# Performance work log

Measured on AMD Instinct MI355X. Metric: run time of the kernel, lower is better.

Reference implementation:

```python
import jax, jax.numpy as jnp
import numpy as np

H = 1024          # hidden_size
A = 8             # num_actions
T = 64            # timesteps
N = 256           # batch (num envs)


def _gru_cell(x, h, Wih, Whh, bih, bhh):
    # torch.nn.GRUCell math; gate order (r, z, n)
    gi = x @ Wih.T + bih           # [N, 3H]
    gh = h @ Whh.T + bhh           # [N, 3H]
    i_r, i_z, i_n = jnp.split(gi, 3, axis=1)
    h_r, h_z, h_n = jnp.split(gh, 3, axis=1)
    r = jax.nn.sigmoid(i_r + h_r)
    z = jax.nn.sigmoid(i_z + h_z)
    n = jnp.tanh(i_n + r * h_n)
    return (1.0 - z) * n + z * h


def setup_inputs() -> dict:
    key = jax.random.key(0)
    ks = jax.random.split(key, 12)
    s = 0.02
    return {
        "c": jax.random.normal(ks[0], (T * N, H), jnp.float32),
        "hxs": jax.random.normal(ks[1], (N, 3 * H), jnp.float32),
        "masks": jnp.ones((T * N, 1), jnp.float32),
        "prev_action_one_hot": jnp.zeros((T * N, A), jnp.float32).at[jnp.arange(T * N), jax.random.randint(ks[2], (T * N,), 0, A)].set(1.0),
        "h_gru_Wih": s * jax.random.normal(ks[3], (3 * H, H), jnp.float32),
        "h_gru_Whh": s * jax.random.normal(ks[4], (3 * H, H), jnp.float32),
        "h_gru_bih": jnp.zeros((3 * H,), jnp.float32),
        "h_gru_bhh": jnp.zeros((3 * H,), jnp.float32),
        "f_gru_Wih": s * jax.random.normal(ks[5], (3 * H, H), jnp.float32),
        "f_gru_Whh": s * jax.random.normal(ks[6], (3 * H, H), jnp.float32),
        "f_gru_bih": jnp.zeros((3 * H,), jnp.float32),
        "f_gru_bhh": jnp.zeros((3 * H,), jnp.float32),
        "p_W": s * jax.random.normal(ks[7], (2 * H, 2 * H + A), jnp.float32),
        "p_b": jnp.zeros((2 * H,), jnp.float32),
        "q_W": s * jax.random.normal(ks[8], (2 * H, 2 * H + A), jnp.float32),
        "q_b": jnp.zeros((2 * H,), jnp.float32),
    }


def reference(c, hxs, masks, prev_action_one_hot,
              h_gru_Wih, h_gru_Whh, h_gru_bih, h_gru_bhh,
              f_gru_Wih, f_gru_Whh, f_gru_bih, f_gru_bhh,
              p_W, p_b, q_W, q_b):
    c3 = c.reshape(T, N, H)
    m3 = masks.reshape(T, N, 1)
    a3 = prev_action_one_hot.reshape(T, N, A)
    f0 = hxs[:, :H]
    h0 = hxs[:, H:2 * H]
    q0 = hxs[:, 2 * H:]

    def step(carry, xs):
        f, h, q_mu = carry
        c_t, m_t, a_t = xs
        p_in = jnp.concatenate([h, q_mu, a_t], axis=1) * m_t
        p_dist = p_in @ p_W.T + p_b                     # [N, 2H]
        p_mu = p_dist[:, :H]
        q_in = jnp.concatenate([f, c_t, a_t], axis=1) * m_t
        q_dist = q_in @ q_W.T + q_b                     # [N, 2H]
        q_mu_new = q_dist[:, :H]
        f_new = _gru_cell(c_t, f * m_t, f_gru_Wih, f_gru_Whh, f_gru_bih, f_gru_bhh)
        h_new = _gru_cell(p_mu, h * m_t, h_gru_Wih, h_gru_Whh, h_gru_bih, h_gru_bhh)
        return (f_new, h_new, q_mu_new), (p_dist, q_dist)

    (f, h, q_mu), (p_all, q_all) = jax.lax.scan(step, (f0, h0, q0), (c3, m3, a3))
    acc_p = p_all.reshape(T * N, 2 * H)
    acc_q = q_all.reshape(T * N, 2 * H)
    hxs_out = jnp.concatenate([f, h, q_mu], axis=1)
    return acc_p, acc_q, hxs_out
```

## Files before the change

kernel.cpp:

```cpp
#include <hip/hip_runtime.h>
#include <math.h>

typedef __attribute__((ext_vector_type(8))) __bf16 bf16x8;
typedef __attribute__((ext_vector_type(4))) float f32x4;

constexpr int H = 1024, T = 64, NB = 256, TWOH = 2048, THREEH = 3072;
constexpr long long OFF_Q  = 33554432LL;
constexpr long long OFF_HX = 67108864LL;
constexpr int LA = 6;

constexpr int R_PWH = 0, R_PWQ = 2048, R_QWF = 4096, R_QWC = 6144,
              R_FWIH = 8192, R_FWHH = 11264, R_HWIH = 14336, R_HWHH = 17408;

#define LD4(p) (*reinterpret_cast<const float4*>(p))

__device__ __forceinline__ float sigf(float x) { return 1.0f / (1.0f + expf(-x)); }

__device__ __forceinline__ void gload16(const void* g, void* l) {
    __builtin_amdgcn_global_load_lds(
        (const __attribute__((address_space(1))) uint32_t*)g,
        (__attribute__((address_space(3))) uint32_t*)l, 16, 0, 0);
}

__device__ __forceinline__ void st_bf_swz(__bf16* base, int n, int k, float v) {
    base[(size_t)n * 1024 + (((k >> 3) ^ (n & 7)) << 3) + (k & 7)] = (__bf16)v;
}

__device__ __forceinline__ void swz_rc(int i, int NR, int& rt, int& ct) {
    const int k = i & 7;
    const int m = i >> 3;
    ct = k + 8 * (m / NR);
    rt = m % NR;
}

#define FRAGOFF(rloc, gl) (((rloc) << 7) + ((((gl)) ^ ((rloc) & 7)) << 4))

template<int RT>
__device__ __forceinline__ void stage_tile(const char* g, char* l, int kb, int tid) {
    #pragma unroll
    for (int i = 0; i < RT / 32; ++i) {
        const int L = i * 4096 + tid * 16;
        gload16(g + (size_t)(L >> 7) * 2048 + (size_t)kb * 128 + (L & 127), l + L);
    }
}

__device__ __forceinline__ void mm128(
    int tid, char* sA, char* sB,
    const char* A, const char* B,
    f32x4 (&acc)[2][4])
{
    const int lane = tid & 63, w = tid >> 6;
    const int l15 = lane & 15, lg = lane >> 4;
    const int wr = w >> 1, wc = w & 1;
    int aoff[2][2], boff[4][2];
    #pragma unroll
    for (int fr = 0; fr < 2; ++fr)
        #pragma unroll
        for (int kk = 0; kk < 2; ++kk)
            aoff[fr][kk] = FRAGOFF(wr * 32 + fr * 16 + l15, kk * 4 + lg);
    #pragma unroll
    for (int fc = 0; fc < 4; ++fc)
        #pragma unroll
        for (int kk = 0; kk < 2; ++kk)
            boff[fc][kk] = FRAGOFF(wc * 64 + fc * 16 + l15, kk * 4 + lg);

    stage_tile<64>(A, sA, 0, tid);
    stage_tile<128>(B, sB, 0, tid);
    stage_tile<64>(A, sA + 8192, 1, tid);
    stage_tile<128>(B, sB + 16384, 1, tid);
    for (int kb = 0; kb < 16; ++kb) {
        const int kn = kb + 2;
        if (kn < 16) {
            const int bo = kn % 3;
            stage_tile<64>(A, sA + bo * 8192, kn, tid);
            stage_tile<128>(B, sB + bo * 16384, kn, tid);
            asm volatile("s_waitcnt vmcnt(12)" ::: "memory");
        } else if (kb + 1 < 16) {
            asm volatile("s_waitcnt vmcnt(6)" ::: "memory");
        } else {
            asm volatile("s_waitcnt vmcnt(0)" ::: "memory");
        }
        __builtin_amdgcn_s_barrier();
        __builtin_amdgcn_sched_barrier(0);
        const int bc = kb % 3;
        char* Ab = sA + bc * 8192;
        char* Bb = sB + bc * 16384;
        bf16x8 af[2][2], bv[4][2];
        #pragma unroll
        for (int fr = 0; fr < 2; ++fr)
            #pragma unroll
            for (int kk = 0; kk < 2; ++kk)
                af[fr][kk] = *reinterpret_cast<const bf16x8*>(Ab + aoff[fr][kk]);
        #pragma unroll
        for (int fc = 0; fc < 4; ++fc)
            #pragma unroll
            for (int kk = 0; kk < 2; ++kk)
                bv[fc][kk] = *reinterpret_cast<const bf16x8*>(Bb + boff[fc][kk]);
        __builtin_amdgcn_s_setprio(1);
        #pragma unroll
        for (int kk = 0; kk < 2; ++kk)
            #pragma unroll
            for (int fr = 0; fr < 2; ++fr)
                #pragma unroll
                for (int fc = 0; fc < 4; ++fc)
                    acc[fr][fc] = __builtin_amdgcn_mfma_f32_16x16x32_bf16(
                        af[fr][kk], bv[fc][kk], acc[fr][fc], 0, 0, 0);
        __builtin_amdgcn_s_setprio(0);
        __builtin_amdgcn_s_barrier();
        __builtin_amdgcn_sched_barrier(0);
    }
}

__device__ __forceinline__ void mm32g1(
    int tid, char* sA, char* sB,
    const char* A, const char* Bg,
    f32x4 (&aR)[2], f32x4 (&aZ)[2], f32x4 (&aN)[2])
{
    const int lane = tid & 63, w = tid >> 6;
    const int l15 = lane & 15, lg = lane >> 4;
    const int wr = w >> 1, wc = w & 1;
    int aoff[2], boff[2][2];
    #pragma unroll
    for (int kk = 0; kk < 2; ++kk)
        aoff[kk] = FRAGOFF(wr * 16 + l15, kk * 4 + lg);
    #pragma unroll
    for (int fc = 0; fc < 2; ++fc)
        #pragma unroll
        for (int kk = 0; kk < 2; ++kk)
            boff[fc][kk] = FRAGOFF(wc * 32 + fc * 16 + l15, kk * 4 + lg);

    auto stg = [&](int buf, int kb) {
        stage_tile<32>(A, sA + buf * 4096, kb, tid);
        #pragma unroll
        for (int g = 0; g < 3; ++g)
            stage_tile<64>(Bg + (size_t)g * 2097152, sB + buf * 24576 + g * 8192, kb, tid);
    };
    stg(0, 0);
    for (int kb = 0; kb < 16; ++kb) {
        if (kb + 1 < 16) {
            stg((kb + 1) & 1, kb + 1);
            asm volatile("s_waitcnt vmcnt(7)" ::: "memory");
        } else {
            asm volatile("s_waitcnt vmcnt(0)" ::: "memory");
        }
        __builtin_amdgcn_s_barrier();
        __builtin_amdgcn_sched_barrier(0);
        char* Ab = sA + (kb & 1) * 4096;
        char* Bb = sB + (kb & 1) * 24576;
        bf16x8 af[2];
        #pragma unroll
        for (int kk = 0; kk < 2; ++kk)
            af[kk] = *reinterpret_cast<const bf16x8*>(Ab + aoff[kk]);
        bf16x8 bvr[2][2], bvz[2][2], bvn[2][2];
        #pragma unroll
        for (int fc = 0; fc < 2; ++fc)
            #pragma unroll
            for (int kk = 0; kk < 2; ++kk) {
                bvr[fc][kk] = *reinterpret_cast<const bf16x8*>(Bb + boff[fc][kk]);
                bvz[fc][kk] = *reinterpret_cast<const bf16x8*>(Bb + 8192 + boff[fc][kk]);
                bvn[fc][kk] = *reinterpret_cast<const bf16x8*>(Bb + 16384 + boff[fc][kk]);
            }
        __builtin_amdgcn_s_setprio(1);
        #pragma unroll
        for (int kk = 0; kk < 2; ++kk)
            #pragma unroll
            for (int fc = 0; fc < 2; ++fc) {
                aR[fc] = __builtin_amdgcn_mfma_f32_16x16x32_bf16(af[kk], bvr[fc][kk], aR[fc], 0, 0, 0);
                aZ[fc] = __builtin_amdgcn_mfma_f32_16x16x32_bf16(af[kk], bvz[fc][kk], aZ[fc], 0, 0, 0);
                aN[fc] = __builtin_amdgcn_mfma_f32_16x16x32_bf16(af[kk], bvn[fc][kk], aN[fc], 0, 0, 0);
            }
        __builtin_amdgcn_s_setprio(0);
        __builtin_amdgcn_s_barrier();
        __builtin_amdgcn_sched_barrier(0);
    }
}

__device__ __forceinline__ void do_xq(int slice, int i, int tid, char* sA, char* sB,
    const char* cbfB, const char* Wb, const float* act, const float* qW, float* out)
{
    const int lane = tid & 63, w = tid >> 6;
    const int l15 = lane & 15, lg = lane >> 4;
    const int wr = w >> 1, wc = w & 1;
    int rt, ct; swz_rc(i, 4, rt, ct);
    const int row0 = rt * 64, col0 = ct * 128;
    const size_t grow0 = (size_t)slice * NB + row0;
    f32x4 acc[2][4] = {};
    mm128(tid, sA, sB, cbfB + grow0 * 2048, Wb + (size_t)(R_QWC + col0) * 2048, acc);
    #pragma unroll
    for (int fc = 0; fc < 4; ++fc) {
        const int gc = col0 + wc * 64 + fc * 16 + l15;
        const float* wp = qW + (size_t)gc * 2056 + 2048;
        float4 x0 = LD4(wp), x1 = LD4(wp + 4);
        #pragma unroll
        for (int fr = 0; fr < 2; ++fr)
            #pragma unroll
            for (int j = 0; j < 4; ++j) {
                const size_t n = grow0 + wr * 32 + fr * 16 + lg * 4 + j;
                const float* ar = act + n * 8;
                float4 a0 = LD4(ar), a1 = LD4(ar + 4);
                float dot = a0.x * x0.x + a0.y * x0.y + a0.z * x0.z + a0.w * x0.w
                          + a1.x * x1.x + a1.y * x1.y + a1.z * x1.z + a1.w * x1.w;
                out[OFF_Q + n * TWOH + gc] = acc[fr][fc][j] + dot;
            }
    }
}

__device__ __forceinline__ void do_gf(int slice, int i, int tid, char* sA, char* sB,
    const char* cbfB, const char* Wb, __bf16* Gfb)
{
    const int lane = tid & 63, w = tid >> 6;
    const int l15 = lane & 15, lg = lane >> 4;
    const int wr = w >> 1, wc = w & 1;
    int rt, ct; swz_rc(i, 4, rt, ct);
    const int row0 = rt * 64, col0 = ct * 128;
    f32x4 acc[2][4] = {};
    mm128(tid, sA, sB, cbfB + ((size_t)slice * NB + row0) * 2048,
          Wb + (size_t)(R_FWIH + col0) * 2048, acc);
    __bf16* gdst = Gfb + (size_t)(slice & 7) * NB * THREEH;
    #pragma unroll
    for (int fc = 0; fc < 4; ++fc) {
        const int gc = col0 + wc * 64 + fc * 16 + l15;
        #pragma unroll
        for (int fr = 0; fr < 2; ++fr)
            #pragma unroll
            for (int j = 0; j < 4; ++j) {
                const int n = row0 + wr * 32 + fr * 16 + lg * 4 + j;
                gdst[(size_t)n * THREEH + gc] = (__bf16)acc[fr][fc][j];
            }
    }
}

__device__ __forceinline__ void do_pq(int tt, int i, int tid, char* sA, char* sB,
    const __bf16* qmu_t, const char* Wb, const float* masks, const float* act,
    const float* pW, const float* pb, float* out)
{
    const int lane = tid & 63, w = tid >> 6;
    const int l15 = lane & 15, lg = lane >> 4;
    const int wr = w >> 1, wc = w & 1;
    int rt, ct; swz_rc(i, 4, rt, ct);
    const int row0 = rt * 64, col0 = ct * 128;
    f32x4 acc[2][4] = {};
    mm128(tid, sA, sB, (const char*)qmu_t + (size_t)row0 * 2048,
          Wb + (size_t)(R_PWQ + col0) * 2048, acc);
    const float* mrow = masks + (size_t)tt * NB;
    float* ob = out + (size_t)tt * NB * TWOH;
    #pragma unroll
    for (int fc = 0; fc < 4; ++fc) {
        const int gc = col0 + wc * 64 + fc * 16 + l15;
        const float* wp = pW + (size_t)gc * 2056 + 2048;
        float4 x0 = LD4(wp), x1 = LD4(wp + 4);
        const float bb = pb[gc];
        #pragma unroll
        for (int fr = 0; fr < 2; ++fr)
            #pragma unroll
            for (int j = 0; j < 4; ++j) {
                const int n = row0 + wr * 32 + fr * 16 + lg * 4 + j;
                const float* ar = act + ((size_t)tt * NB + n) * 8;
                float4 a0 = LD4(ar), a1 = LD4(ar + 4);
                float dot = a0.x * x0.x + a0.y * x0.y + a0.z * x0.z + a0.w * x0.w
                          + a1.x * x1.x + a1.y * x1.y + a1.z * x1.z + a1.w * x1.w;
                ob[(size_t)n * TWOH + gc] = acc[fr][fc][j] + mrow[n] * dot + bb;
            }
    }
}

__global__ __launch_bounds__(256) void wcvt_k(
    const float* __restrict__ pW, const float* __restrict__ qW,
    const float* __restrict__ fWih, const float* __restrict__ fWhh,
    const float* __restrict__ hWih, const float* __restrict__ hWhh,
    __bf16* __restrict__ Wbf)
{
    const long i = (long)blockIdx.x * 256 + threadIdx.x;
    const int row = (int)(i >> 7);
    const int G   = (int)i & 127;
    const float* src; int stride; int koff = 0; int r;
    if (row < 2048)       { src = pW;   stride = 2056; koff = 0;    r = row; }
    else if (row < 4096)  { src = pW;   stride = 2056; koff = 1024; r = row - 2048; }
    else if (row < 6144)  { src = qW;   stride = 2056; koff = 0;    r = row - 4096; }
    else if (row < 8192)  { src = qW;   stride = 2056; koff = 1024; r = row - 6144; }
    else if (row < 11264) { src = fWih; stride = 1024; r = row - 8192; }
    else if (row < 14336) { src = fWhh; stride = 1024; r = row - 11264; }
    else if (row < 17408) { src = hWih; stride = 1024; r = row - 14336; }
    else                  { src = hWhh; stride = 1024; r = row - 17408; }
    const float* p = src + (long)r * stride + koff + G * 8;
    float4 a = LD4(p), b = LD4(p + 4);
    bf16x8 v;
    v[0] = (__bf16)a.x; v[1] = (__bf16)a.y; v[2] = (__bf16)a.z; v[3] = (__bf16)a.w;
    v[4] = (__bf16)b.x; v[5] = (__bf16)b.y; v[6] = (__bf16)b.z; v[7] = (__bf16)b.w;
    *reinterpret_cast<bf16x8*>(Wbf + (size_t)row * 1024 + ((G ^ (row & 7)) << 3)) = v;
}

__global__ __launch_bounds__(256) void ccvt_k(const float* __restrict__ c,
                                              __bf16* __restrict__ cbf) {
    const long i = (long)blockIdx.x * 256 + threadIdx.x;
    const int row = (int)(i >> 7);
    const int G   = (int)i & 127;
    const float* p = c + (size_t)row * 1024 + G * 8;
    float4 a = LD4(p), b = LD4(p + 4);
    bf16x8 v;
    v[0] = (__bf16)a.x; v[1] = (__bf16)a.y; v[2] = (__bf16)a.z; v[3] = (__bf16)a.w;
    v[4] = (__bf16)b.x; v[5] = (__bf16)b.y; v[6] = (__bf16)b.z; v[7] = (__bf16)b.w;
    *reinterpret_cast<bf16x8*>(cbf + (size_t)row * 1024 + ((G ^ (row & 7)) << 3)) = v;
}

__global__ __launch_bounds__(256) void init2_k(
    const float* __restrict__ hxs, const float* __restrict__ masks,
    float* __restrict__ fst0, float* __restrict__ hst0,
    __bf16* __restrict__ fbm0, __bf16* __restrict__ hbm0, __bf16* __restrict__ qmub0)
{
    const int idx = blockIdx.x * 256 + threadIdx.x;
    const int arr = idx >> 15;
    const int g   = idx & 32767;
    const int n   = g >> 7;
    const int G   = g & 127;
    const float m0 = masks[n];
    const float* p = hxs + (size_t)n * THREEH + arr * 1024 + G * 8;
    float4 a = LD4(p), b = LD4(p + 4);
    __bf16* dstB = arr == 0 ? fbm0 : (arr == 1 ? hbm0 : qmub0);
    bf16x8 v;
    v[0] = (__bf16)(a.x * m0); v[1] = (__bf16)(a.y * m0);
    v[2] = (__bf16)(a.z * m0); v[3] = (__bf16)(a.w * m0);
    v[4] = (__bf16)(b.x * m0); v[5] = (__bf16)(b.y * m0);
    v[6] = (__bf16)(b.z * m0); v[7] = (__bf16)(b.w * m0);
    *reinterpret_cast<bf16x8*>(dstB + (size_t)n * 1024 + ((G ^ (n & 7)) << 3)) = v;
    if (arr < 2) {
        float* dstF = arr == 0 ? fst0 : hst0;
        *reinterpret_cast<float4*>(dstF + (size_t)n * 1024 + G * 8) = a;
        *reinterpret_cast<float4*>(dstF + (size_t)n * 1024 + G * 8 + 4) = b;
    }
}

__global__ __launch_bounds__(256) void pre_k(
    const char* __restrict__ cbfB, const char* __restrict__ Wb,
    const float* __restrict__ act, const float* __restrict__ qW,
    const __bf16* __restrict__ qmb0, const float* __restrict__ masks,
    const float* __restrict__ pW, const float* __restrict__ pb,
    __bf16* __restrict__ Gfb, float* __restrict__ out)
{
    __shared__ char smem[73728];
    if (blockIdx.x < LA * 160) {
        const int s = blockIdx.x / 160;
        const int i = blockIdx.x % 160;
        if (i < 64) do_xq(s, i, threadIdx.x, smem, smem + 24576, cbfB, Wb, act, qW, out);
        else        do_gf(s, i - 64, threadIdx.x, smem, smem + 24576, cbfB, Wb, Gfb);
    } else {
        do_pq(0, blockIdx.x - LA * 160, threadIdx.x, smem, smem + 24576,
              qmb0, Wb, masks, act, pW, pb, out);
    }
}

__global__ __launch_bounds__(256) void k1_k(
    int t,
    const __bf16* __restrict__ hbm, const __bf16* __restrict__ fbm,
    __bf16* __restrict__ qmubN,
    const float* __restrict__ masks, const float* __restrict__ act,
    const float* __restrict__ qb, const float* __restrict__ qW,
    const char* __restrict__ Wb,
    __bf16* __restrict__ pmub, float* __restrict__ Shh,
    const __bf16* __restrict__ Gfb,
    const float* __restrict__ fbih, const float* __restrict__ fbhh,
    const float* __restrict__ fstF, float* __restrict__ fstN, __bf16* __restrict__ fbmN,
    float* __restrict__ out)
{
    __shared__ char smem[73728];
    char* sA = smem;
    char* sB = smem + 24576;
    const int tid = threadIdx.x;
    const int lane = tid & 63, w = tid >> 6;
    const int l15 = lane & 15, lg = lane >> 4;
    const int wr = w >> 1, wc = w & 1;
    const float* mrow = masks + (size_t)t * NB;
    const float* mn   = masks + (size_t)(t + 1 < T ? t + 1 : t) * NB;
    int b = blockIdx.x;

    if (b < 64) {
        int rt, ct; swz_rc(b, 4, rt, ct);
        const int row0 = rt * 64, col0 = ct * 128;
        f32x4 acc[2][4] = {};
        mm128(tid, sA, sB, (const char*)hbm + (size_t)row0 * 2048,
              Wb + (size_t)(R_PWH + col0) * 2048, acc);
        float* ob = out + (size_t)t * NB * TWOH;
        #pragma unroll
        for (int fc = 0; fc < 4; ++fc) {
            const int gc = col0 + wc * 64 + fc * 16 + l15;
            #pragma unroll
            for (int fr = 0; fr < 2; ++fr)
                #pragma unroll
                for (int j = 0; j < 4; ++j) {
                    const int n = row0 + wr * 32 + fr * 16 + lg * 4 + j;
                    const float v = ob[(size_t)n * TWOH + gc] + acc[fr][fc][j];
                    ob[(size_t)n * TWOH + gc] = v;
                    if (gc < 1024) st_bf_swz(pmub, n, gc, v);
                }
        }
    } else if (b < 128) {
        int rt, ct; swz_rc(b - 64, 4, rt, ct);
        const int row0 = rt * 64, col0 = ct * 128;
        f32x4 acc[2][4] = {};
        mm128(tid, sA, sB, (const char*)fbm + (size_t)row0 * 2048,
              Wb + (size_t)(R_QWF + col0) * 2048, acc);
        float* ob = out + OFF_Q + (size_t)t * NB * TWOH;
        #pragma unroll
        for (int fc = 0; fc < 4; ++fc) {
            const int gc = col0 + wc * 64 + fc * 16 + l15;
            const float bb = qb[gc];
            #pragma unroll
            for (int fr = 0; fr < 2; ++fr)
                #pragma unroll
                for (int j = 0; j < 4; ++j) {
                    const int n = row0 + wr * 32 + fr * 16 + lg * 4 + j;
                    const float xq = ob[(size_t)n * TWOH + gc];
                    float v = acc[fr][fc][j] + mrow[n] * xq + bb;
                    ob[(size_t)n * TWOH + gc] = v;
                    if (gc < 1024) st_bf_swz(qmubN, n, gc, v * mn[n]);
                }
        }
    } else if (b < 224) {
        int rt, ct; swz_rc(b - 128, 4, rt, ct);
        const int row0 = rt * 64, col0 = ct * 128;
        f32x4 acc[2][4] = {};
        mm128(tid, sA, sB, (const char*)hbm + (size_t)row0 * 2048,
              Wb + (size_t)(R_HWHH + col0) * 2048, acc);
        #pragma unroll
        for (int fc = 0; fc < 4; ++fc) {
            const int gc = col0 + wc * 64 + fc * 16 + l15;
            #pragma unroll
            for (int fr = 0; fr < 2; ++fr)
                #pragma unroll
                for (int j = 0; j < 4; ++j) {
                    const int n = row0 + wr * 32 + fr * 16 + lg * 4 + j;
                    Shh[(size_t)n * THREEH + gc] = acc[fr][fc][j];
                }
        }
    } else {
        int rt, ct; swz_rc(b - 224, 8, rt, ct);
        const int row0 = rt * 32, col0 = ct * 64;
        f32x4 aR[2] = {}, aZ[2] = {}, aN[2] = {};
        mm32g1(tid, sA, sB, (const char*)fbm + (size_t)row0 * 2048,
               Wb + (size_t)(R_FWHH + col0) * 2048, aR, aZ, aN);
        const __bf16* gsl = Gfb + (size_t)(t & 7) * NB * THREEH;
        #pragma unroll
        for (int fc = 0; fc < 2; ++fc) {
            const int col = col0 + wc * 32 + fc * 16 + l15;
            const float br  = fbih[col] + fbhh[col];
            const float bz  = fbih[col + 1024] + fbhh[col + 1024];
            const float bni = fbih[col + 2048], bnh = fbhh[col + 2048];
            #pragma unroll
            for (int j = 0; j < 4; ++j) {
                const int n = row0 + wr * 16 + lg * 4 + j;
                const float gfr = (float)gsl[(size_t)n * THREEH + col];
                const float gfz = (float)gsl[(size_t)n * THREEH + col + 1024];
                const float gfn = (float)gsl[(size_t)n * THREEH + col + 2048];
                const float rg = sigf(gfr + aR[fc][j] + br);
                const float zg = sigf(gfz + aZ[fc][j] + bz);
                const float ng = tanhf(gfn + bni + rg * (aN[fc][j] + bnh));
                const float fm = fstF[(size_t)n * 1024 + col] * mrow[n];
                const float o = (1.f - zg) * ng + zg * fm;
                fstN[(size_t)n * 1024 + col] = o;
                st_bf_swz(fbmN, n, col, o * mn[n]);
            }
        }
    }
}

__global__ __launch_bounds__(256) void k2_k(
    int t,
    const __bf16* __restrict__ pmub, const __bf16* __restrict__ qmubN,
    const char* __restrict__ cbfB,
    const float* __restrict__ Shh,
    const float* __restrict__ hstF, float* __restrict__ hstN, __bf16* __restrict__ hbmN,
    const char* __restrict__ Wb,
    const float* __restrict__ hbih, const float* __restrict__ hbhh,
    const float* __restrict__ masks, const float* __restrict__ act,
    const float* __restrict__ pW, const float* __restrict__ pb,
    const float* __restrict__ qW,
    __bf16* __restrict__ Gfb, float* __restrict__ out)
{
    __shared__ char smem[73728];
    char* sA = smem;
    char* sB = smem + 24576;
    const int tid = threadIdx.x;
    const int lane = tid & 63, w = tid >> 6;
    const int l15 = lane & 15, lg = lane >> 4;
    const int wr = w >> 1, wc = w & 1;
    const float* mrow = masks + (size_t)t * NB;
    const float* mn   = masks + (size_t)(t + 1 < T ? t + 1 : t) * NB;
    const int b = blockIdx.x;

    if (b < 128) {
        int rt, ct; swz_rc(b, 8, rt, ct);
        const int row0 = rt * 32, col0 = ct * 64;
        f32x4 aR[2] = {}, aZ[2] = {}, aN[2] = {};
        mm32g1(tid, sA, sB, (const char*)pmub + (size_t)row0 * 2048,
               Wb + (size_t)(R_HWIH + col0) * 2048, aR, aZ, aN);
        #pragma unroll
        for (int fc = 0; fc < 2; ++fc) {
            const int col = col0 + wc * 32 + fc * 16 + l15;
            const float bri = hbih[col],        brh = hbhh[col];
            const float bzi = hbih[col + 1024], bzh = hbhh[col + 1024];
            const float bni = hbih[col + 2048], bnh = hbhh[col + 2048];
            #pragma unroll
            for (int j = 0; j < 4; ++j) {
                const int n = row0 + wr * 16 + lg * 4 + j;
                const float ghr = Shh[(size_t)n * THREEH + col];
                const float ghz = Shh[(size_t)n * THREEH + col + 1024];
                const float ghn = Shh[(size_t)n * THREEH + col + 2048];
                const float rg = sigf(aR[fc][j] + bri + ghr + brh);
                const float zg = sigf(aZ[fc][j] + bzi + ghz + bzh);
                const float ng = tanhf(aN[fc][j] + bni + rg * (ghn + bnh));
                const float hm = hstF[(size_t)n * 1024 + col] * mrow[n];
                const float o = (1.f - zg) * ng + zg * hm;
                hstN[(size_t)n * 1024 + col] = o;
                st_bf_swz(hbmN, n, col, o * mn[n]);
            }
        }
    } else if (b < 192) {
        if (t + 1 < T)
            do_pq(t + 1, b - 128, tid, sA, sB, qmubN, Wb, masks, act, pW, pb, out);
    } else if (b < 256) {
        if (t + LA < T)
            do_xq(t + LA, b - 192, tid, sA, sB, cbfB, Wb, act, qW, out);
    } else {
        if (t + LA < T)
            do_gf(t + LA, b - 256, tid, sA, sB, cbfB, Wb, Gfb);
    }
}

__global__ __launch_bounds__(256) void write_hxs_k(const float* __restrict__ fS,
                                                   const float* __restrict__ hS,
                                                   float* out) {
    const int i = blockIdx.x * 256 + threadIdx.x;
    const int n = i / THREEH;
    const int j = i - n * THREEH;
    float v;
    if (j < H)          v = fS[(size_t)n * H + j];
    else if (j < TWOH)  v = hS[(size_t)n * H + (j - H)];
    else                v = out[OFF_Q + ((size_t)(T - 1) * NB + n) * TWOH + (j - TWOH)];
    out[OFF_HX + i] = v;
}

extern "C" void kernel_launch(void* const* d_in, const int* in_sizes, int n_in,
                              void* d_out, int out_size, void* d_ws, size_t ws_size,
                              hipStream_t stream) {
    (void)in_sizes; (void)n_in; (void)out_size; (void)ws_size;

    const float* c     = (const float*)d_in[0];
    const float* hxs   = (const float*)d_in[1];
    const float* masks = (const float*)d_in[2];
    const float* act   = (const float*)d_in[3];
    const float* hWih  = (const float*)d_in[4];
    const float* hWhh  = (const float*)d_in[5];
    const float* hbih  = (const float*)d_in[6];
    const float* hbhh  = (const float*)d_in[7];
    const float* fWih  = (const float*)d_in[8];
    const float* fWhh  = (const float*)d_in[9];
    const float* fbih  = (const float*)d_in[10];
    const float* fbhh  = (const float*)d_in[11];
    const float* pW    = (const float*)d_in[12];
    const float* pb    = (const float*)d_in[13];
    const float* qW    = (const float*)d_in[14];
    const float* qb    = (const float*)d_in[15];

    float* out = (float*)d_out;
    char*  wsb = (char*)d_ws;

    __bf16* Wbf  = (__bf16*)(wsb);
    __bf16* cbf  = (__bf16*)(wsb + 41943040LL);
    float*  fst[2] = { (float*)(wsb + 75497472LL), (float*)(wsb + 76546048LL) };
    float*  hst[2] = { (float*)(wsb + 77594624LL), (float*)(wsb + 78643200LL) };
    __bf16* fbm[2] = { (__bf16*)(wsb + 79691776LL), (__bf16*)(wsb + 80216064LL) };
    __bf16* hbm[2] = { (__bf16*)(wsb + 80740352LL), (__bf16*)(wsb + 81264640LL) };
    __bf16* qmb[2] = { (__bf16*)(wsb + 81788928LL), (__bf16*)(wsb + 82313216LL) };
    __bf16* pmub   = (__bf16*)(wsb + 82837504LL);
    float*  Shh    = (float*)(wsb + 83361792LL);
    __bf16* Gfb    = (__bf16*)(wsb + 86507520LL);
    const char* Wb   = (const char*)Wbf;
    const char* cbfB = (const char*)cbf;

    wcvt_k <<<dim3(10240), dim3(256), 0, stream>>>(pW, qW, fWih, fWhh, hWih, hWhh, Wbf);
    ccvt_k <<<dim3(8192),  dim3(256), 0, stream>>>(c, cbf);
    init2_k<<<dim3(384),   dim3(256), 0, stream>>>(hxs, masks, fst[0], hst[0],
                                                   fbm[0], hbm[0], qmb[0]);
    pre_k  <<<dim3(LA * 160 + 64), dim3(256), 0, stream>>>(
        cbfB, Wb, act, qW, qmb[0], masks, pW, pb, Gfb, out);

    for (int t = 0; t < T; ++t) {
        const int cur = t & 1, nxt = cur ^ 1;
        k1_k<<<dim3(352), dim3(256), 0, stream>>>(
            t, hbm[cur], fbm[cur], qmb[nxt],
            masks, act, qb, qW, Wb, pmub, Shh, Gfb,
            fbih, fbhh, fst[cur], fst[nxt], fbm[nxt], out);
        k2_k<<<dim3(352), dim3(256), 0, stream>>>(
            t, pmub, qmb[nxt], cbfB, Shh,
            hst[cur], hst[nxt], hbm[nxt],
            Wb, hbih, hbhh, masks, act, pW, pb, qW, Gfb, out);
    }

    write_hxs_k<<<dim3(3072), dim3(256), 0, stream>>>(fst[0], hst[0], out);
}
```

Baseline: 2.144 ms.

## Widen GEMM tiles to 64x256 with 512-thread blocks and pair GRU tasks

```diff
diff --git a/kernel.cpp b/kernel.cpp
--- a/kernel.cpp
+++ b/kernel.cpp
@@ -26,13 +26,6 @@
     base[(size_t)n * 1024 + (((k >> 3) ^ (n & 7)) << 3) + (k & 7)] = (__bf16)v;
 }
 
-__device__ __forceinline__ void swz_rc(int i, int NR, int& rt, int& ct) {
-    const int k = i & 7;
-    const int m = i >> 3;
-    ct = k + 8 * (m / NR);
-    rt = m % NR;
-}
-
 #define FRAGOFF(rloc, gl) (((rloc) << 7) + ((((gl)) ^ ((rloc) & 7)) << 4))
 
 template<int RT>
@@ -44,14 +37,23 @@
     }
 }
 
-__device__ __forceinline__ void mm128(
+template<int RT>
+__device__ __forceinline__ void stage512(const char* g, char* l, int kb, int tid) {
+    #pragma unroll
+    for (int i = 0; i < RT / 64; ++i) {
+        const int L = i * 8192 + tid * 16;
+        gload16(g + (size_t)(L >> 7) * 2048 + (size_t)kb * 128 + (L & 127), l + L);
+    }
+}
+
+__device__ __forceinline__ void mm256(
     int tid, char* sA, char* sB,
     const char* A, const char* B,
     f32x4 (&acc)[2][4])
 {
     const int lane = tid & 63, w = tid >> 6;
     const int l15 = lane & 15, lg = lane >> 4;
-    const int wr = w >> 1, wc = w & 1;
+    const int wr = w >> 2, wc = w & 3;
     int aoff[2][2], boff[4][2];
     #pragma unroll
     for (int fr = 0; fr < 2; ++fr)
@@ -64,19 +66,19 @@
         for (int kk = 0; kk < 2; ++kk)
             boff[fc][kk] = FRAGOFF(wc * 64 + fc * 16 + l15, kk * 4 + lg);
 
-    stage_tile<64>(A, sA, 0, tid);
-    stage_tile<128>(B, sB, 0, tid);
-    stage_tile<64>(A, sA + 8192, 1, tid);
-    stage_tile<128>(B, sB + 16384, 1, tid);
+    stage512<64>(A, sA, 0, tid);
+    stage512<256>(B, sB, 0, tid);
+    stage512<64>(A, sA + 8192, 1, tid);
+    stage512<256>(B, sB + 32768, 1, tid);
     for (int kb = 0; kb < 16; ++kb) {
         const int kn = kb + 2;
         if (kn < 16) {
             const int bo = kn % 3;
-            stage_tile<64>(A, sA + bo * 8192, kn, tid);
-            stage_tile<128>(B, sB + bo * 16384, kn, tid);
-            asm volatile("s_waitcnt vmcnt(12)" ::: "memory");
+            stage512<64>(A, sA + bo * 8192, kn, tid);
+            stage512<256>(B, sB + bo * 32768, kn, tid);
+            asm volatile("s_waitcnt vmcnt(10)" ::: "memory");
         } else if (kb + 1 < 16) {
-            asm volatile("s_waitcnt vmcnt(6)" ::: "memory");
+            asm volatile("s_waitcnt vmcnt(5)" ::: "memory");
         } else {
             asm volatile("s_waitcnt vmcnt(0)" ::: "memory");
         }
@@ -84,7 +86,7 @@
         __builtin_amdgcn_sched_barrier(0);
         const int bc = kb % 3;
         char* Ab = sA + bc * 8192;
-        char* Bb = sB + bc * 16384;
+        char* Bb = sB + bc * 32768;
         bf16x8 af[2][2], bv[4][2];
         #pragma unroll
         for (int fr = 0; fr < 2; ++fr)
@@ -176,16 +178,17 @@
 }
 
 __device__ __forceinline__ void do_xq(int slice, int i, int tid, char* sA, char* sB,
-    const char* cbfB, const char* Wb, const float* act, const float* qW, float* out)
+    const char* cbfB, const char* Wb, const float* act, const float* qW, float* out,
+    bool wr_en)
 {
     const int lane = tid & 63, w = tid >> 6;
     const int l15 = lane & 15, lg = lane >> 4;
-    const int wr = w >> 1, wc = w & 1;
-    int rt, ct; swz_rc(i, 4, rt, ct);
-    const int row0 = rt * 64, col0 = ct * 128;
+    const int wr = w >> 2, wc = w & 3;
+    const int row0 = (i >> 3) * 64, col0 = (i & 7) * 256;
     const size_t grow0 = (size_t)slice * NB + row0;
     f32x4 acc[2][4] = {};
-    mm128(tid, sA, sB, cbfB + grow0 * 2048, Wb + (size_t)(R_QWC + col0) * 2048, acc);
+    mm256(tid, sA, sB, cbfB + grow0 * 2048, Wb + (size_t)(R_QWC + col0) * 2048, acc);
+    if (!wr_en) return;
     #pragma unroll
     for (int fc = 0; fc < 4; ++fc) {
         const int gc = col0 + wc * 64 + fc * 16 + l15;
@@ -206,16 +209,16 @@
 }
 
 __device__ __forceinline__ void do_gf(int slice, int i, int tid, char* sA, char* sB,
-    const char* cbfB, const char* Wb, __bf16* Gfb)
+    const char* cbfB, const char* Wb, __bf16* Gfb, bool wr_en)
 {
     const int lane = tid & 63, w = tid >> 6;
     const int l15 = lane & 15, lg = lane >> 4;
-    const int wr = w >> 1, wc = w & 1;
-    int rt, ct; swz_rc(i, 4, rt, ct);
-    const int row0 = rt * 64, col0 = ct * 128;
+    const int wr = w >> 2, wc = w & 3;
+    const int row0 = (i / 12) * 64, col0 = (i % 12) * 256;
     f32x4 acc[2][4] = {};
-    mm128(tid, sA, sB, cbfB + ((size_t)slice * NB + row0) * 2048,
+    mm256(tid, sA, sB, cbfB + ((size_t)slice * NB + row0) * 2048,
           Wb + (size_t)(R_FWIH + col0) * 2048, acc);
+    if (!wr_en) return;
     __bf16* gdst = Gfb + (size_t)(slice & 7) * NB * THREEH;
     #pragma unroll
     for (int fc = 0; fc < 4; ++fc) {
@@ -232,16 +235,16 @@
 
 __device__ __forceinline__ void do_pq(int tt, int i, int tid, char* sA, char* sB,
     const __bf16* qmu_t, const char* Wb, const float* masks, const float* act,
-    const float* pW, const float* pb, float* out)
+    const float* pW, const float* pb, float* out, bool wr_en)
 {
     const int lane = tid & 63, w = tid >> 6;
     const int l15 = lane & 15, lg = lane >> 4;
-    const int wr = w >> 1, wc = w & 1;
-    int rt, ct; swz_rc(i, 4, rt, ct);
-    const int row0 = rt * 64, col0 = ct * 128;
+    const int wr = w >> 2, wc = w & 3;
+    const int row0 = (i >> 3) * 64, col0 = (i & 7) * 256;
     f32x4 acc[2][4] = {};
-    mm128(tid, sA, sB, (const char*)qmu_t + (size_t)row0 * 2048,
+    mm256(tid, sA, sB, (const char*)qmu_t + (size_t)row0 * 2048,
           Wb + (size_t)(R_PWQ + col0) * 2048, acc);
+    if (!wr_en) return;
     const float* mrow = masks + (size_t)tt * NB;
     float* ob = out + (size_t)tt * NB * TWOH;
     #pragma unroll
@@ -330,26 +333,27 @@
     }
 }
 
-__global__ __launch_bounds__(256) void pre_k(
+__global__ __launch_bounds__(512) void pre_k(
     const char* __restrict__ cbfB, const char* __restrict__ Wb,
     const float* __restrict__ act, const float* __restrict__ qW,
     const __bf16* __restrict__ qmb0, const float* __restrict__ masks,
     const float* __restrict__ pW, const float* __restrict__ pb,
     __bf16* __restrict__ Gfb, float* __restrict__ out)
 {
-    __shared__ char smem[73728];
-    if (blockIdx.x < LA * 160) {
-        const int s = blockIdx.x / 160;
-        const int i = blockIdx.x % 160;
-        if (i < 64) do_xq(s, i, threadIdx.x, smem, smem + 24576, cbfB, Wb, act, qW, out);
-        else        do_gf(s, i - 64, threadIdx.x, smem, smem + 24576, cbfB, Wb, Gfb);
+    __shared__ char smem[122880];
+    const int tid = threadIdx.x;
+    const int b = blockIdx.x;
+    if (b < LA * 80) {
+        const int s = b / 80;
+        const int i = b % 80;
+        if (i < 32) do_xq(s, i, tid, smem, smem + 24576, cbfB, Wb, act, qW, out, true);
+        else        do_gf(s, i - 32, tid, smem, smem + 24576, cbfB, Wb, Gfb, true);
     } else {
-        do_pq(0, blockIdx.x - LA * 160, threadIdx.x, smem, smem + 24576,
-              qmb0, Wb, masks, act, pW, pb, out);
-    }
-}
-
-__global__ __launch_bounds__(256) void k1_k(
+        do_pq(0, b - LA * 80, tid, smem, smem + 24576, qmb0, Wb, masks, act, pW, pb, out, true);
+    }
+}
+
+__global__ __launch_bounds__(512) void k1_k(
     int t,
     const __bf16* __restrict__ hbm, const __bf16* __restrict__ fbm,
     __bf16* __restrict__ qmubN,
@@ -362,81 +366,88 @@
     const float* __restrict__ fstF, float* __restrict__ fstN, __bf16* __restrict__ fbmN,
     float* __restrict__ out)
 {
-    __shared__ char smem[73728];
-    char* sA = smem;
-    char* sB = smem + 24576;
+    __shared__ char smem[122880];
     const int tid = threadIdx.x;
-    const int lane = tid & 63, w = tid >> 6;
-    const int l15 = lane & 15, lg = lane >> 4;
-    const int wr = w >> 1, wc = w & 1;
     const float* mrow = masks + (size_t)t * NB;
     const float* mn   = masks + (size_t)(t + 1 < T ? t + 1 : t) * NB;
-    int b = blockIdx.x;
-
-    if (b < 64) {
-        int rt, ct; swz_rc(b, 4, rt, ct);
-        const int row0 = rt * 64, col0 = ct * 128;
-        f32x4 acc[2][4] = {};
-        mm128(tid, sA, sB, (const char*)hbm + (size_t)row0 * 2048,
-              Wb + (size_t)(R_PWH + col0) * 2048, acc);
-        float* ob = out + (size_t)t * NB * TWOH;
-        #pragma unroll
-        for (int fc = 0; fc < 4; ++fc) {
-            const int gc = col0 + wc * 64 + fc * 16 + l15;
-            #pragma unroll
-            for (int fr = 0; fr < 2; ++fr)
+    const int b = blockIdx.x;
+
+    if (b < 112) {
+        char* sA = smem;
+        char* sB = smem + 24576;
+        const int lane = tid & 63, w = tid >> 6;
+        const int l15 = lane & 15, lg = lane >> 4;
+        const int wr = w >> 2, wc = w & 3;
+        if (b < 32) {
+            const int row0 = (b >> 3) * 64, col0 = (b & 7) * 256;
+            f32x4 acc[2][4] = {};
+            mm256(tid, sA, sB, (const char*)hbm + (size_t)row0 * 2048,
+                  Wb + (size_t)(R_PWH + col0) * 2048, acc);
+            float* ob = out + (size_t)t * NB * TWOH;
+            #pragma unroll
+            for (int fc = 0; fc < 4; ++fc) {
+                const int gc = col0 + wc * 64 + fc * 16 + l15;
                 #pragma unroll
-                for (int j = 0; j < 4; ++j) {
-                    const int n = row0 + wr * 32 + fr * 16 + lg * 4 + j;
-                    const float v = ob[(size_t)n * TWOH + gc] + acc[fr][fc][j];
-                    ob[(size_t)n * TWOH + gc] = v;
-                    if (gc < 1024) st_bf_swz(pmub, n, gc, v);
-                }
-        }
-    } else if (b < 128) {
-        int rt, ct; swz_rc(b - 64, 4, rt, ct);
-        const int row0 = rt * 64, col0 = ct * 128;
-        f32x4 acc[2][4] = {};
-        mm128(tid, sA, sB, (const char*)fbm + (size_t)row0 * 2048,
-              Wb + (size_t)(R_QWF + col0) * 2048, acc);
-        float* ob = out + OFF_Q + (size_t)t * NB * TWOH;
-        #pragma unroll
-        for (int fc = 0; fc < 4; ++fc) {
-            const int gc = col0 + wc * 64 + fc * 16 + l15;
-            const float bb = qb[gc];
-            #pragma unroll
-            for (int fr = 0; fr < 2; ++fr)
+                for (int fr = 0; fr < 2; ++fr)
+                    #pragma unroll
+                    for (int j = 0; j < 4; ++j) {
+                        const int n = row0 + wr * 32 + fr * 16 + lg * 4 + j;
+                        const float v = ob[(size_t)n * TWOH + gc] + acc[fr][fc][j];
+                        ob[(size_t)n * TWOH + gc] = v;
+                        if (gc < 1024) st_bf_swz(pmub, n, gc, v);
+                    }
+            }
+        } else if (b < 64) {
+            const int i = b - 32;
+            const int row0 = (i >> 3) * 64, col0 = (i & 7) * 256;
+            f32x4 acc[2][4] = {};
+            mm256(tid, sA, sB, (const char*)fbm + (size_t)row0 * 2048,
+                  Wb + (size_t)(R_QWF + col0) * 2048, acc);
+            float* ob = out + OFF_Q + (size_t)t * NB * TWOH;
+            #pragma unroll
+            for (int fc = 0; fc < 4; ++fc) {
+                const int gc = col0 + wc * 64 + fc * 16 + l15;
+                const float bb = qb[gc];
                 #pragma unroll
-                for (int j = 0; j < 4; ++j) {
-                    const int n = row0 + wr * 32 + fr * 16 + lg * 4 + j;
-                    const float xq = ob[(size_t)n * TWOH + gc];
-                    float v = acc[fr][fc][j] + mrow[n] * xq + bb;
-                    ob[(size_t)n * TWOH + gc] = v;
-                    if (gc < 1024) st_bf_swz(qmubN, n, gc, v * mn[n]);
-                }
-        }
-    } else if (b < 224) {
-        int rt, ct; swz_rc(b - 128, 4, rt, ct);
-        const int row0 = rt * 64, col0 = ct * 128;
-        f32x4 acc[2][4] = {};
-        mm128(tid, sA, sB, (const char*)hbm + (size_t)row0 * 2048,
-              Wb + (size_t)(R_HWHH + col0) * 2048, acc);
-        #pragma unroll
-        for (int fc = 0; fc < 4; ++fc) {
-            const int gc = col0 + wc * 64 + fc * 16 + l15;
-            #pragma unroll
-            for (int fr = 0; fr < 2; ++fr)
+                for (int fr = 0; fr < 2; ++fr)
+                    #pragma unroll
+                    for (int j = 0; j < 4; ++j) {
+                        const int n = row0 + wr * 32 + fr * 16 + lg * 4 + j;
+                        const float xq = ob[(size_t)n * TWOH + gc];
+                        float v = acc[fr][fc][j] + mrow[n] * xq + bb;
+                        ob[(size_t)n * TWOH + gc] = v;
+                        if (gc < 1024) st_bf_swz(qmubN, n, gc, v * mn[n]);
+                    }
+            }
+        } else {
+            const int i = b - 64;
+            const int row0 = (i / 12) * 64, col0 = (i % 12) * 256;
+            f32x4 acc[2][4] = {};
+            mm256(tid, sA, sB, (const char*)hbm + (size_t)row0 * 2048,
+                  Wb + (size_t)(R_HWHH + col0) * 2048, acc);
+            #pragma unroll
+            for (int fc = 0; fc < 4; ++fc) {
+                const int gc = col0 + wc * 64 + fc * 16 + l15;
                 #pragma unroll
-                for (int j = 0; j < 4; ++j) {
-                    const int n = row0 + wr * 32 + fr * 16 + lg * 4 + j;
-                    Shh[(size_t)n * THREEH + gc] = acc[fr][fc][j];
-                }
+                for (int fr = 0; fr < 2; ++fr)
+                    #pragma unroll
+                    for (int j = 0; j < 4; ++j) {
+                        const int n = row0 + wr * 32 + fr * 16 + lg * 4 + j;
+                        Shh[(size_t)n * THREEH + gc] = acc[fr][fc][j];
+                    }
+            }
         }
     } else {
-        int rt, ct; swz_rc(b - 224, 8, rt, ct);
-        const int row0 = rt * 32, col0 = ct * 64;
+        const int half = tid >> 8;
+        const int ht = tid & 255;
+        char* base = smem + half * 57344;
+        const int task = (b - 112) * 2 + half;
+        const int row0 = (task >> 4) * 32, col0 = (task & 15) * 64;
+        const int lane = ht & 63, w = ht >> 6;
+        const int l15 = lane & 15, lg = lane >> 4;
+        const int wr = w >> 1, wc = w & 1;
         f32x4 aR[2] = {}, aZ[2] = {}, aN[2] = {};
-        mm32g1(tid, sA, sB, (const char*)fbm + (size_t)row0 * 2048,
+        mm32g1(ht, base, base + 8192, (const char*)fbm + (size_t)row0 * 2048,
                Wb + (size_t)(R_FWHH + col0) * 2048, aR, aZ, aN);
         const __bf16* gsl = Gfb + (size_t)(t & 7) * NB * THREEH;
         #pragma unroll
@@ -463,7 +474,7 @@
     }
 }
 
-__global__ __launch_bounds__(256) void k2_k(
+__global__ __launch_bounds__(512) void k2_k(
     int t,
     const __bf16* __restrict__ pmub, const __bf16* __restrict__ qmubN,
     const char* __restrict__ cbfB,
@@ -476,22 +487,23 @@
     const float* __restrict__ qW,
     __bf16* __restrict__ Gfb, float* __restrict__ out)
 {
-    __shared__ char smem[73728];
-    char* sA = smem;
-    char* sB = smem + 24576;
+    __shared__ char smem[122880];
     const int tid = threadIdx.x;
-    const int lane = tid & 63, w = tid >> 6;
-    const int l15 = lane & 15, lg = lane >> 4;
-    const int wr = w >> 1, wc = w & 1;
     const float* mrow = masks + (size_t)t * NB;
     const float* mn   = masks + (size_t)(t + 1 < T ? t + 1 : t) * NB;
     const int b = blockIdx.x;
 
-    if (b < 128) {
-        int rt, ct; swz_rc(b, 8, rt, ct);
-        const int row0 = rt * 32, col0 = ct * 64;
+    if (b < 64) {
+        const int half = tid >> 8;
+        const int ht = tid & 255;
+        char* base = smem + half * 57344;
+        const int task = b * 2 + half;
+        const int row0 = (task >> 4) * 32, col0 = (task & 15) * 64;
+        const int lane = ht & 63, w = ht >> 6;
+        const int l15 = lane & 15, lg = lane >> 4;
+        const int wr = w >> 1, wc = w & 1;
         f32x4 aR[2] = {}, aZ[2] = {}, aN[2] = {};
-        mm32g1(tid, sA, sB, (const char*)pmub + (size_t)row0 * 2048,
+        mm32g1(ht, base, base + 8192, (const char*)pmub + (size_t)row0 * 2048,
                Wb + (size_t)(R_HWIH + col0) * 2048, aR, aZ, aN);
         #pragma unroll
         for (int fc = 0; fc < 2; ++fc) {
@@ -514,15 +526,18 @@
                 st_bf_swz(hbmN, n, col, o * mn[n]);
             }
         }
-    } else if (b < 192) {
-        if (t + 1 < T)
-            do_pq(t + 1, b - 128, tid, sA, sB, qmubN, Wb, masks, act, pW, pb, out);
-    } else if (b < 256) {
-        if (t + LA < T)
-            do_xq(t + LA, b - 192, tid, sA, sB, cbfB, Wb, act, qW, out);
+    } else if (b < 96) {
+        const bool wr_en = (t + 1 < T);
+        const int tt = wr_en ? t + 1 : t;
+        do_pq(tt, b - 64, tid, smem, smem + 24576, qmubN, Wb, masks, act, pW, pb, out, wr_en);
+    } else if (b < 128) {
+        const bool wr_en = (t + LA < T);
+        const int s = wr_en ? t + LA : T - 1;
+        do_xq(s, b - 96, tid, smem, smem + 24576, cbfB, Wb, act, qW, out, wr_en);
     } else {
-        if (t + LA < T)
-            do_gf(t + LA, b - 256, tid, sA, sB, cbfB, Wb, Gfb);
+        const bool wr_en = (t + LA < T);
+        const int s = wr_en ? t + LA : T - 1;
+        do_gf(s, b - 128, tid, smem, smem + 24576, cbfB, Wb, Gfb, wr_en);
     }
 }
 
@@ -581,16 +596,16 @@
     ccvt_k <<<dim3(8192),  dim3(256), 0, stream>>>(c, cbf);
     init2_k<<<dim3(384),   dim3(256), 0, stream>>>(hxs, masks, fst[0], hst[0],
                                                    fbm[0], hbm[0], qmb[0]);
-    pre_k  <<<dim3(LA * 160 + 64), dim3(256), 0, stream>>>(
+    pre_k  <<<dim3(LA * 80 + 32), dim3(512), 0, stream>>>(
         cbfB, Wb, act, qW, qmb[0], masks, pW, pb, Gfb, out);
 
     for (int t = 0; t < T; ++t) {
         const int cur = t & 1, nxt = cur ^ 1;
-        k1_k<<<dim3(352), dim3(256), 0, stream>>>(
+        k1_k<<<dim3(176), dim3(512), 0, stream>>>(
             t, hbm[cur], fbm[cur], qmb[nxt],
             masks, act, qb, qW, Wb, pmub, Shh, Gfb,
             fbih, fbhh, fst[cur], fst[nxt], fbm[nxt], out);
-        k2_k<<<dim3(352), dim3(256), 0, stream>>>(
+        k2_k<<<dim3(176), dim3(512), 0, stream>>>(
             t, pmub, qmb[nxt], cbfB, Shh,
             hst[cur], hst[nxt], hbm[nxt],
             Wb, hbih, hbhh, masks, act, pW, pb, qW, Gfb, out);
```

Result: slower. 2.530 ms (+18.0%).
